# Optimization experiments

Hardware: AMD Instinct MI355X
Metric: run time of the kernel (lower is better)

## Reference

```python
import jax, jax.numpy as jnp
import numpy as np

N_K = 20000; N_E = 50000; N_U = 100000; EMB = 128
E_UND = 200000; E_EK = 400000; E_EU = 600000


def _gat(h, W, a, src, dst, n):
    """RCD GraphLayer: single-head GAT with edge softmax over incoming edges."""
    z = h @ W                                  # [N, d]
    d = z.shape[1]
    el = z @ a[:d]                             # src contribution to attn logit
    er = z @ a[d:]                             # dst contribution
    e = jax.nn.leaky_relu(el[src] + er[dst], 0.01)   # [E]
    m = jax.ops.segment_max(e, dst, num_segments=n)
    m = jnp.where(jnp.isfinite(m), m, 0.0)     # guard zero-degree nodes
    ex = jnp.exp(e - m[dst])
    s = jax.ops.segment_sum(ex, dst, num_segments=n)
    alpha = ex / s[dst]                        # per-dst softmax weights [E]
    return jax.ops.segment_sum(alpha[:, None] * z[src], dst, num_segments=n)


def setup_inputs() -> dict:
    key = jax.random.key(0)
    ks = jax.random.split(key, 32)
    sc = 1.0 / np.sqrt(EMB)
    inp = {
        'kn_emb': jax.random.normal(ks[0], (N_K, EMB), jnp.float32),
        'exer_emb': jax.random.normal(ks[1], (N_E, EMB), jnp.float32),
        'all_stu_emb': jax.random.normal(ks[2], (N_U, EMB), jnp.float32),
        'und_src': jax.random.randint(ks[3], (E_UND,), 0, N_K),
        'und_dst': jax.random.randint(ks[4], (E_UND,), 0, N_K),
        'ek_src': jax.random.randint(ks[5], (E_EK,), 0, N_E),
        'ek_dst': jax.random.randint(ks[6], (E_EK,), 0, N_K),
        'eu_src': jax.random.randint(ks[7], (E_EU,), 0, N_E),
        'eu_dst': jax.random.randint(ks[8], (E_EU,), 0, N_U),
        'W_und': jax.random.normal(ks[9], (EMB, EMB), jnp.float32) * sc,
        'a_und': jax.random.normal(ks[10], (2 * EMB,), jnp.float32) * sc,
        'W_ek': jax.random.normal(ks[11], (EMB, EMB), jnp.float32) * sc,
        'a_ek': jax.random.normal(ks[12], (2 * EMB,), jnp.float32) * sc,
        'W_ke': jax.random.normal(ks[13], (EMB, EMB), jnp.float32) * sc,
        'a_ke': jax.random.normal(ks[14], (2 * EMB,), jnp.float32) * sc,
        'W_eu': jax.random.normal(ks[15], (EMB, EMB), jnp.float32) * sc,
        'a_eu': jax.random.normal(ks[16], (2 * EMB,), jnp.float32) * sc,
        'W_ue': jax.random.normal(ks[17], (EMB, EMB), jnp.float32) * sc,
        'a_ue': jax.random.normal(ks[18], (2 * EMB,), jnp.float32) * sc,
        'k_fc2_w': jax.random.normal(ks[19], (2 * EMB,), jnp.float32) * sc,
        'k_fc2_b': jnp.zeros((1,), jnp.float32),
        'k_fc3_w': jax.random.normal(ks[20], (2 * EMB,), jnp.float32) * sc,
        'k_fc3_b': jnp.zeros((1,), jnp.float32),
        'e_fc1_w': jax.random.normal(ks[21], (2 * EMB,), jnp.float32) * sc,
        'e_fc1_b': jnp.zeros((1,), jnp.float32),
        'e_fc2_w': jax.random.normal(ks[22], (2 * EMB,), jnp.float32) * sc,
        'e_fc2_b': jnp.zeros((1,), jnp.float32),
    }
    return inp


def reference(kn_emb, exer_emb, all_stu_emb, und_src, und_dst, ek_src, ek_dst,
              eu_src, eu_dst, W_und, a_und, W_ek, a_ek, W_ke, a_ke, W_eu, a_eu,
              W_ue, a_ue, k_fc2_w, k_fc2_b, k_fc3_w, k_fc3_b, e_fc1_w, e_fc1_b,
              e_fc2_w, e_fc2_b):
    d = EMB
    # 1) undirected GAT on knowledge graph
    k_und = _gat(kn_emb, W_und, a_und, und_src, und_dst, N_K)
    # 2) exercise<->knowledge graphs on concatenated [exer; kn] nodes
    ek_nodes = jnp.concatenate([exer_emb, kn_emb], axis=0)
    e2k = _gat(ek_nodes, W_ek, a_ek, ek_src, ek_dst + N_E, N_E + N_K)
    k2e = _gat(ek_nodes, W_ke, a_ke, ek_dst + N_E, ek_src, N_E + N_K)
    # 3) exercise<->student graphs on concatenated [exer; stu] nodes
    eu_nodes = jnp.concatenate([exer_emb, all_stu_emb], axis=0)
    e2u = _gat(eu_nodes, W_eu, a_eu, eu_src, eu_dst + N_E, N_E + N_U)
    u2e = _gat(eu_nodes, W_ue, a_ue, eu_dst + N_E, eu_src, N_E + N_U)
    # knowledge fusion: attention-weighted residual combination
    A = kn_emb; C = k_und; D = e2k[N_E:]
    s2 = A @ k_fc2_w[:d] + C @ k_fc2_w[d:] + k_fc2_b[0]
    s3 = A @ k_fc3_w[:d] + D @ k_fc3_w[d:] + k_fc3_b[0]
    sk = jax.nn.softmax(jnp.stack([s2, s3], axis=1), axis=1)
    kn_out = A + sk[:, 0:1] * C + sk[:, 1:2] * D
    # exercise fusion
    Ae = exer_emb; B = k2e[:N_E]; Ce = u2e[:N_E]
    s1 = Ae @ e_fc1_w[:d] + B @ e_fc1_w[d:] + e_fc1_b[0]
    s2e = Ae @ e_fc2_w[:d] + Ce @ e_fc2_w[d:] + e_fc2_b[0]
    se = jax.nn.softmax(jnp.stack([s1, s2e], axis=1), axis=1)
    exer_out = Ae + se[:, 0:1] * B + se[:, 1:2] * Ce
    # student residual
    stu_out = all_stu_emb + e2u[N_E:]
    return (kn_out, exer_out, stu_out)
```

## Files before the change

### kernel.cpp

```cpp
#include <hip/hip_runtime.h>

#define N_K 20000
#define N_E 50000
#define N_U 100000
#define E_TOT 2200000
#define N_TOT 240000
#define KB1 0
#define KB2 20000
#define KB3 40000
#define KB4 90000
#define KB5 190000
#define NBKT 726
#define EPB 8192
#define NBLKA 269
#define APAD 272
#define KN_B 1250
#define EX_B 3125
#define ST_B 6250

typedef unsigned short u16;
typedef unsigned int u32;
typedef __bf16 bf16x8 __attribute__((ext_vector_type(8)));
typedef float f32x4 __attribute__((ext_vector_type(4)));

__device__ __forceinline__ float bf2f(u16 v){
    union { u32 u; float f; } x; x.u = ((u32)v) << 16; return x.f;
}
__device__ __forceinline__ u16 f2bf(float f){
    union { float f; u32 u; } x; x.f = f;
    u32 r = x.u + 0x7FFFu + ((x.u >> 16) & 1u);
    return (u16)(r >> 16);
}
__device__ __forceinline__ float leaky_exp(float x){
    x = x >= 0.f ? x : 0.01f*x;
    return __expf(x);
}

__device__ __forceinline__ int bucket_of(int key){
    if (key < 20000)  return key >> 8;
    if (key < 40000)  return 79  + ((key - 20000) >> 7);
    if (key < 90000)  return 236 + ((key - 40000) >> 9);
    if (key < 190000) return 334 + ((key - 90000) >> 9);
    return 530 + ((key - 190000) >> 8);
}
__device__ __forceinline__ int local_of(int key){
    if (key < 20000)  return key & 255;
    if (key < 40000)  return (key - 20000) & 127;
    if (key < 90000)  return (key - 40000) & 511;
    if (key < 190000) return (key - 90000) & 511;
    return (key - 190000) & 255;
}
__device__ __forceinline__ void bucket_info(int b, int& kb, int& w, int& r){
    if (b < 79){       r=0; kb = b << 8;                 w = min(256, 20000  - kb); }
    else if (b < 236){ r=1; kb = 20000 + ((b-79)  << 7); w = min(128, 40000  - kb); }
    else if (b < 334){ r=2; kb = 40000 + ((b-236) << 9); w = min(512, 90000  - kb); }
    else if (b < 530){ r=3; kb = 90000 + ((b-334) << 9); w = min(512, 190000 - kb); }
    else {             r=4; kb = 190000 + ((b-530) << 8); w = min(256, 240000 - kb); }
}
__device__ __forceinline__ int edge_key(int e,
    const int* ud, const int* es, const int* ed, const int* vs, const int* vd){
    if (e < 200000)  return ud[e];
    if (e < 600000)  return 20000  + ed[e-200000];
    if (e < 1000000) return 40000  + es[e-600000];
    if (e < 1600000) return 90000  + vd[e-1000000];
    return 190000 + vs[e-1600000];
}
__device__ __forceinline__ int edge_src(int e,
    const int* us, const int* es, const int* ed, const int* vs, const int* vd){
    if (e < 200000)  return us[e];
    if (e < 600000)  return es[e-200000];
    if (e < 1000000) return ed[e-600000];
    if (e < 1600000) return vs[e-1000000];
    return vd[e-1600000];
}

__global__ __launch_bounds__(256) void prep_w(
    const float* W0, const float* W1, const float* W2, const float* W3, const float* W4,
    const float* a0, const float* a1, const float* a2, const float* a3, const float* a4,
    float* __restrict__ vecs, u16* __restrict__ Wf)
{
    int bid = blockIdx.x;
    if (bid < 320){
        int o = bid*4 + (threadIdx.x >> 6);
        int lane = threadIdx.x & 63;
        int which = o / 640, rem = o - which*640, g = rem >> 7, k = rem & 127;
        const float* W = g==0?W0:g==1?W1:g==2?W2:g==3?W3:W4;
        const float* a = g==0?a0:g==1?a1:g==2?a2:g==3?a3:a4;
        const float* av = a + which*128;
        int c = lane*2;
        float s = W[k*128 + c]*av[c] + W[k*128 + c + 1]*av[c+1];
        #pragma unroll
        for (int m = 32; m; m >>= 1) s += __shfl_xor(s, m);
        if (lane == 0) vecs[(which*5 + g)*128 + k] = s;
    } else {
        int t = (bid - 320)*256 + threadIdx.x;
        int g = t / 2048, i = t - g*2048;
        const float* W = g==0?W0:g==1?W1:g==2?W2:g==3?W3:W4;
        int lane = i & 63, tt = i >> 6, ks = tt & 3, ct = tt >> 2;
        int kbase = ks*32 + (lane>>4)*8;
        int c = ct*16 + (lane&15);
        #pragma unroll
        for (int j = 0; j < 8; ++j)
            Wf[g*16384 + i*8 + j] = f2bf(W[(kbase+j)*128 + c]);
    }
}

template<int WBF>
__global__ __launch_bounds__(256) void conv_all(
    const float* __restrict__ kn, const float* __restrict__ exer, const float* __restrict__ stu,
    u16* __restrict__ knb, u16* __restrict__ exerb, u16* __restrict__ stub,
    const float* __restrict__ vecs,
    float* __restrict__ el1, float* __restrict__ el2, float* __restrict__ el3,
    float* __restrict__ el4, float* __restrict__ el5, float* __restrict__ erc)
{
    int w = (int)((blockIdx.x*(u32)blockDim.x + threadIdx.x) >> 6);
    int lane = threadIdx.x & 63;
    if (w >= 170000) return;
    const float* h; u16* hb; int local, nd;
    const float *v0,*v1,*v2,*v3;
    float *o0,*o1,*o2,*o3;
    if (w < 20000){
        local = w; h = kn; hb = knb; nd = 4;
        v0=vecs+0;    v1=vecs+640;  v2=vecs+768;  v3=vecs+256;
        o0=el1; o1=erc+KB1; o2=erc+KB2; o3=el3;
    } else if (w < 70000){
        local = w - 20000; h = exer; hb = exerb; nd = 4;
        v0=vecs+128;  v1=vecs+896;  v2=vecs+384;  v3=vecs+1152;
        o0=el2; o1=erc+KB3; o2=el4; o3=erc+KB5;
    } else {
        local = w - 70000; h = stu; hb = stub; nd = 2;
        v0=vecs+1024; v1=vecs+512;  v2=vecs;      v3=vecs;
        o0=erc+KB4; o1=el5; o2=nullptr; o3=nullptr;
    }
    float2 hv = *(const float2*)(h + (size_t)local*128 + lane*2);
    if (WBF)
        *(u32*)(hb + (size_t)local*128 + lane*2) = (u32)f2bf(hv.x) | ((u32)f2bf(hv.y) << 16);
    int c = lane*2;
    float d0 = hv.x*v0[c] + hv.y*v0[c+1];
    float d1 = hv.x*v1[c] + hv.y*v1[c+1];
    float d2 = hv.x*v2[c] + hv.y*v2[c+1];
    float d3 = hv.x*v3[c] + hv.y*v3[c+1];
    #pragma unroll
    for (int o = 32; o; o >>= 1){
        d0 += __shfl_xor(d0, o); d1 += __shfl_xor(d1, o);
        d2 += __shfl_xor(d2, o); d3 += __shfl_xor(d3, o);
    }
    if (lane == 0){
        o0[local] = d0; o1[local] = d1;
        if (nd == 4){ o2[local] = d2; o3[local] = d3; }
    }
}

__global__ __launch_bounds__(256) void bkt_hist(
    const int* __restrict__ ud, const int* __restrict__ es, const int* __restrict__ ed,
    const int* __restrict__ vs, const int* __restrict__ vd, int* __restrict__ hist)
{
    __shared__ int h[NBKT];
    for (int i = threadIdx.x; i < NBKT; i += 256) h[i] = 0;
    __syncthreads();
    int base = blockIdx.x * EPB;
    #pragma unroll 4
    for (int it = 0; it < EPB/256; ++it){
        int e = base + it*256 + threadIdx.x;
        if (e < E_TOT){
            int key = edge_key(e, ud, es, ed, vs, vd);
            atomicAdd(&h[bucket_of(key)], 1);
        }
    }
    __syncthreads();
    for (int i = threadIdx.x; i < NBKT; i += 256)
        hist[i*APAD + blockIdx.x] = h[i];
}

__global__ __launch_bounds__(512) void bkt_scan1(int* __restrict__ hist, int* __restrict__ btot)
{
    __shared__ int sm[512];
    int t = threadIdx.x;
    int v = (t < NBLKA) ? hist[blockIdx.x*APAD + t] : 0;
    sm[t] = v; __syncthreads();
    #pragma unroll
    for (int d = 1; d < 512; d <<= 1){
        int x = (t >= d) ? sm[t-d] : 0;
        __syncthreads();
        sm[t] += x;
        __syncthreads();
    }
    if (t < NBLKA) hist[blockIdx.x*APAD + t] = sm[t] - v;
    if (t == 511) btot[blockIdx.x] = sm[511];
}

__global__ __launch_bounds__(1024) void bkt_scan2(const int* __restrict__ btot, int* __restrict__ bbase)
{
    __shared__ int sm[1024];
    int t = threadIdx.x;
    int v = (t < NBKT) ? btot[t] : 0;
    sm[t] = v; __syncthreads();
    #pragma unroll
    for (int d = 1; d < 1024; d <<= 1){
        int x = (t >= d) ? sm[t-d] : 0;
        __syncthreads();
        sm[t] += x;
        __syncthreads();
    }
    if (t < NBKT) bbase[t] = sm[t] - v;
}

__global__ __launch_bounds__(256) void bkt_scatter(
    const int* __restrict__ us, const int* __restrict__ ud,
    const int* __restrict__ es, const int* __restrict__ ed,
    const int* __restrict__ vs, const int* __restrict__ vd,
    const int* __restrict__ hist, const int* __restrict__ bbase,
    const float* __restrict__ el1, const float* __restrict__ el2,
    const float* __restrict__ el3, const float* __restrict__ el4,
    const float* __restrict__ el5, const float* __restrict__ erc,
    uint2* __restrict__ rec)
{
    __shared__ int cur[NBKT];
    for (int i = threadIdx.x; i < NBKT; i += 256)
        cur[i] = bbase[i] + hist[i*APAD + blockIdx.x];
    __syncthreads();
    int base = blockIdx.x * EPB;
    #pragma unroll 4
    for (int it = 0; it < EPB/256; ++it){
        int e = base + it*256 + threadIdx.x;
        if (e < E_TOT){
            int key = edge_key(e, ud, es, ed, vs, vd);
            int src = edge_src(e, us, es, ed, vs, vd);
            const float* el = (e < 200000) ? el1 : (e < 600000) ? el2 :
                              (e < 1000000) ? el3 : (e < 1600000) ? el4 : el5;
            float ev = leaky_exp(el[src] + erc[key]);
            int local = local_of(key);
            int pos = atomicAdd(&cur[bucket_of(key)], 1);
            rec[pos] = make_uint2((u32)src | ((u32)local << 17), __float_as_uint(ev));
        }
    }
}

__global__ __launch_bounds__(512) void bkt_finalize(const uint2* __restrict__ rec,
    const int* __restrict__ bbase, const int* __restrict__ btot,
    int* __restrict__ cnt, int* __restrict__ offA, int2* __restrict__ sorted2)
{
    __shared__ int   h[512];
    __shared__ float s[512];
    __shared__ int   sm[512];
    __shared__ int   curk[512];
    int b = blockIdx.x, t = threadIdx.x;
    int kb, w, r;
    bucket_info(b, kb, w, r);
    h[t] = 0; s[t] = 0.f;
    __syncthreads();
    int start = bbase[b], n = btot[b];
    for (int i = t; i < n; i += 512){
        uint2 rc = rec[start + i];
        int local = (int)(rc.x >> 17);
        atomicAdd(&h[local], 1);
        atomicAdd(&s[local], __uint_as_float(rc.y));
    }
    __syncthreads();
    int hv = h[t];
    if (t < w) cnt[kb + t] = hv;
    sm[t] = hv; __syncthreads();
    #pragma unroll
    for (int d = 1; d < 512; d <<= 1){
        int x = (t >= d) ? sm[t-d] : 0;
        __syncthreads();
        sm[t] += x;
        __syncthreads();
    }
    int pos0 = start + sm[t] - hv;
    if (t < w) offA[kb + t] = pos0;
    curk[t] = pos0;
    __syncthreads();
    for (int i = t; i < n; i += 512){
        uint2 rc = rec[start + i];
        int local = (int)(rc.x >> 17);
        float alpha = __uint_as_float(rc.y) / s[local];
        int pos = atomicAdd(&curk[local], 1);
        sorted2[pos] = make_int2((int)(rc.x & 0x1FFFFu), __float_as_int(alpha));
    }
}

template<int BF>
__global__ __launch_bounds__(256) void agg_gemm_epi(
    const int* __restrict__ cnt, const int* __restrict__ offA, const int2* __restrict__ sorted2,
    const void* __restrict__ hk, const void* __restrict__ he, const void* __restrict__ hs,
    const u16* __restrict__ Wf,
    const float* __restrict__ kfc2w, const float* __restrict__ kfc2b,
    const float* __restrict__ kfc3w, const float* __restrict__ kfc3b,
    const float* __restrict__ efc1w, const float* __restrict__ efc1b,
    const float* __restrict__ efc2w, const float* __restrict__ efc2b,
    float* __restrict__ out)
{
    __shared__ u16 ldsC[16*136];
    __shared__ u16 ldsD[16*136];
    __shared__ float sred2[16], sred3[16], p2s[16], p3s[16];

    int bid = blockIdx.x;
    int wave = threadIdx.x >> 6, lane = threadIdx.x & 63;
    int g = lane >> 4, s = lane & 15;
    int kind, node0, keyC, keyD;
    const void *hC, *hD, *Aseg;
    const u16 *wc, *wd;
    const float *w2, *b2, *w3, *b3;
    float* outp;
    if (bid < KN_B){
        kind=0; node0 = bid*16;
        keyC = KB1 + node0; keyD = KB2 + node0;
        hC = hk; hD = he; Aseg = hk;
        wc = Wf; wd = Wf + 16384;
        w2=kfc2w; b2=kfc2b; w3=kfc3w; b3=kfc3b;
        outp = out;
    } else if (bid < KN_B + EX_B){
        kind=0; node0 = (bid - KN_B)*16;
        keyC = KB3 + node0; keyD = KB5 + node0;
        hC = hk; hD = hs; Aseg = he;
        wc = Wf + 2*16384; wd = Wf + 4*16384;
        w2=efc1w; b2=efc1b; w3=efc2w; b3=efc2b;
        outp = out + (size_t)N_K*128;
    } else {
        kind=1; node0 = (bid - KN_B - EX_B)*16;
        keyC = KB4 + node0; keyD = 0;
        hC = he; hD = nullptr; Aseg = hs;
        wc = Wf + 3*16384; wd = nullptr;
        w2=nullptr; b2=nullptr; w3=nullptr; b3=nullptr;
        outp = out + (size_t)(N_K + N_E)*128;
    }

    int rpw = (kind == 0) ? 8 : 4;
    for (int rr = 0; rr < rpw; rr += 2){
        int cA = wave*rpw + rr;
        int seg = cA >> 4, ndA = cA & 15;
        int keyA = (seg == 0 ? keyC : keyD) + ndA;
        const u16* hb = (const u16*)(seg == 0 ? hC : hD);
        const float4* hf = (const float4*)(seg == 0 ? hC : hD);
        int degA = cnt[keyA],     startA = offA[keyA];
        int degB = cnt[keyA + 1], startB = offA[keyA + 1];
        float aA8[8], aB8[8];
        #pragma unroll
        for (int k = 0; k < 8; ++k){ aA8[k] = 0.f; aB8[k] = 0.f; }

        auto chunk = [&](const int2* sp, float* acc){
            int2 w = sp[g];
            float al = __int_as_float(w.y);
            if (BF){
                uint4 hv = *(const uint4*)(hb + (size_t)w.x*128 + s*8);
                acc[0] = fmaf(al, bf2f((u16)hv.x), acc[0]);
                acc[1] = fmaf(al, bf2f((u16)(hv.x>>16)), acc[1]);
                acc[2] = fmaf(al, bf2f((u16)hv.y), acc[2]);
                acc[3] = fmaf(al, bf2f((u16)(hv.y>>16)), acc[3]);
                acc[4] = fmaf(al, bf2f((u16)hv.z), acc[4]);
                acc[5] = fmaf(al, bf2f((u16)(hv.z>>16)), acc[5]);
                acc[6] = fmaf(al, bf2f((u16)hv.w), acc[6]);
                acc[7] = fmaf(al, bf2f((u16)(hv.w>>16)), acc[7]);
            } else {
                const float4* rp = hf + (size_t)w.x*32 + s*2;
                float4 p0 = rp[0], p1 = rp[1];
                acc[0] = fmaf(al, p0.x, acc[0]); acc[1] = fmaf(al, p0.y, acc[1]);
                acc[2] = fmaf(al, p0.z, acc[2]); acc[3] = fmaf(al, p0.w, acc[3]);
                acc[4] = fmaf(al, p1.x, acc[4]); acc[5] = fmaf(al, p1.y, acc[5]);
                acc[6] = fmaf(al, p1.z, acc[6]); acc[7] = fmaf(al, p1.w, acc[7]);
            }
        };

        int iA = 0, iB = 0;
        while (iA + 4 <= degA && iB + 4 <= degB){
            chunk(sorted2 + startA + iA, aA8);
            chunk(sorted2 + startB + iB, aB8);
            iA += 4; iB += 4;
        }
        for (; iA + 4 <= degA; iA += 4) chunk(sorted2 + startA + iA, aA8);
        for (; iB + 4 <= degB; iB += 4) chunk(sorted2 + startB + iB, aB8);
        int remA = degA - iA;
        if (g < remA) chunk(sorted2 + startA + iA, aA8);
        int remB = degB - iB;
        if (g < remB) chunk(sorted2 + startB + iB, aB8);

        #pragma unroll
        for (int k = 0; k < 8; ++k){
            aA8[k] += __shfl_xor(aA8[k], 16); aA8[k] += __shfl_xor(aA8[k], 32);
            aB8[k] += __shfl_xor(aB8[k], 16); aB8[k] += __shfl_xor(aB8[k], 32);
        }
        u16* ldsSeg = (seg == 0 ? ldsC : ldsD);
        if (lane < 16){
            u32 p0 = (u32)f2bf(aA8[0]) | ((u32)f2bf(aA8[1]) << 16);
            u32 p1 = (u32)f2bf(aA8[2]) | ((u32)f2bf(aA8[3]) << 16);
            u32 p2 = (u32)f2bf(aA8[4]) | ((u32)f2bf(aA8[5]) << 16);
            u32 p3 = (u32)f2bf(aA8[6]) | ((u32)f2bf(aA8[7]) << 16);
            *(uint4*)(ldsSeg + ndA*136 + lane*8) = make_uint4(p0,p1,p2,p3);
            u32 q0 = (u32)f2bf(aB8[0]) | ((u32)f2bf(aB8[1]) << 16);
            u32 q1 = (u32)f2bf(aB8[2]) | ((u32)f2bf(aB8[3]) << 16);
            u32 q2 = (u32)f2bf(aB8[4]) | ((u32)f2bf(aB8[5]) << 16);
            u32 q3 = (u32)f2bf(aB8[6]) | ((u32)f2bf(aB8[7]) << 16);
            *(uint4*)(ldsSeg + (ndA+1)*136 + lane*8) = make_uint4(q0,q1,q2,q3);
        }
    }
    if (threadIdx.x < 16){ sred2[threadIdx.x] = 0.f; sred3[threadIdx.x] = 0.f; }
    __syncthreads();

    int colb = lane & 15, rlo = (lane >> 4)*4;
    const float* Af = (const float*)Aseg;
    const u16*   Ab = (const u16*)Aseg;

    bf16x8 afC[4];
    #pragma unroll
    for (int ks = 0; ks < 4; ++ks)
        afC[ks] = *(const bf16x8*)(ldsC + (lane & 15)*136 + ks*32 + (lane >> 4)*8);
    f32x4 accC[2];
    accC[0] = (f32x4){0.f,0.f,0.f,0.f}; accC[1] = (f32x4){0.f,0.f,0.f,0.f};
    #pragma unroll
    for (int ci = 0; ci < 2; ++ci){
        int ct = wave*2 + ci;
        #pragma unroll
        for (int ks = 0; ks < 4; ++ks){
            bf16x8 bfr = *(const bf16x8*)(wc + ((ct*4+ks)*64 + lane)*8);
            accC[ci] = __builtin_amdgcn_mfma_f32_16x16x32_bf16(afC[ks], bfr, accC[ci], 0, 0, 0);
        }
    }

    if (kind == 1){
        #pragma unroll
        for (int ci = 0; ci < 2; ++ci){
            int ct = wave*2 + ci;
            #pragma unroll
            for (int j = 0; j < 4; ++j){
                size_t idx = (size_t)(node0 + rlo + j)*128 + ct*16 + colb;
                float av = BF ? bf2f(Ab[idx]) : Af[idx];
                outp[idx] = accC[ci][j] + av;
            }
        }
        return;
    }

    bf16x8 afD[4];
    #pragma unroll
    for (int ks = 0; ks < 4; ++ks)
        afD[ks] = *(const bf16x8*)(ldsD + (lane & 15)*136 + ks*32 + (lane >> 4)*8);
    f32x4 accD[2];
    accD[0] = (f32x4){0.f,0.f,0.f,0.f}; accD[1] = (f32x4){0.f,0.f,0.f,0.f};
    #pragma unroll
    for (int ci = 0; ci < 2; ++ci){
        int ct = wave*2 + ci;
        #pragma unroll
        for (int ks = 0; ks < 4; ++ks){
            bf16x8 bfr = *(const bf16x8*)(wd + ((ct*4+ks)*64 + lane)*8);
            accD[ci] = __builtin_amdgcn_mfma_f32_16x16x32_bf16(afD[ks], bfr, accD[ci], 0, 0, 0);
        }
    }

    float aA[2][4];
    float s2p[4] = {0.f,0.f,0.f,0.f}, s3p[4] = {0.f,0.f,0.f,0.f};
    #pragma unroll
    for (int ci = 0; ci < 2; ++ci){
        int ct = wave*2 + ci;
        float w2l = w2[ct*16 + colb], w2h = w2[128 + ct*16 + colb];
        float w3l = w3[ct*16 + colb], w3h = w3[128 + ct*16 + colb];
        #pragma unroll
        for (int j = 0; j < 4; ++j){
            size_t idx = (size_t)(node0 + rlo + j)*128 + ct*16 + colb;
            float av = BF ? bf2f(Ab[idx]) : Af[idx];
            aA[ci][j] = av;
            s2p[j] = fmaf(av, w2l, fmaf(accC[ci][j], w2h, s2p[j]));
            s3p[j] = fmaf(av, w3l, fmaf(accD[ci][j], w3h, s3p[j]));
        }
    }
    #pragma unroll
    for (int m = 8; m; m >>= 1)
        #pragma unroll
        for (int j = 0; j < 4; ++j){
            s2p[j] += __shfl_xor(s2p[j], m);
            s3p[j] += __shfl_xor(s3p[j], m);
        }
    if (colb == 0){
        #pragma unroll
        for (int j = 0; j < 4; ++j){
            atomicAdd(&sred2[rlo + j], s2p[j]);
            atomicAdd(&sred3[rlo + j], s3p[j]);
        }
    }
    __syncthreads();
    if (threadIdx.x < 16){
        float s2 = sred2[threadIdx.x] + b2[0];
        float s3 = sred3[threadIdx.x] + b3[0];
        float mx = fmaxf(s2, s3);
        float e2 = __expf(s2 - mx), e3 = __expf(s3 - mx);
        float inv = 1.f/(e2 + e3);
        p2s[threadIdx.x] = e2*inv;
        p3s[threadIdx.x] = e3*inv;
    }
    __syncthreads();
    #pragma unroll
    for (int ci = 0; ci < 2; ++ci){
        int ct = wave*2 + ci;
        #pragma unroll
        for (int j = 0; j < 4; ++j){
            int row = rlo + j;
            size_t idx = (size_t)(node0 + row)*128 + ct*16 + colb;
            outp[idx] = aA[ci][j] + p2s[row]*accC[ci][j] + p3s[row]*accD[ci][j];
        }
    }
}

extern "C" void kernel_launch(void* const* d_in, const int* in_sizes, int n_in,
                              void* d_out, int out_size, void* d_ws, size_t ws_size,
                              hipStream_t stream)
{
    (void)in_sizes; (void)n_in; (void)out_size;
    const float* kn   = (const float*)d_in[0];
    const float* exer = (const float*)d_in[1];
    const float* stu  = (const float*)d_in[2];
    const int* und_src = (const int*)d_in[3];
    const int* und_dst = (const int*)d_in[4];
    const int* ek_src  = (const int*)d_in[5];
    const int* ek_dst  = (const int*)d_in[6];
    const int* eu_src  = (const int*)d_in[7];
    const int* eu_dst  = (const int*)d_in[8];
    const float* W_und = (const float*)d_in[9];  const float* a_und = (const float*)d_in[10];
    const float* W_ek  = (const float*)d_in[11]; const float* a_ek  = (const float*)d_in[12];
    const float* W_ke  = (const float*)d_in[13]; const float* a_ke  = (const float*)d_in[14];
    const float* W_eu  = (const float*)d_in[15]; const float* a_eu  = (const float*)d_in[16];
    const float* W_ue  = (const float*)d_in[17]; const float* a_ue  = (const float*)d_in[18];
    const float* kfc2w = (const float*)d_in[19]; const float* kfc2b = (const float*)d_in[20];
    const float* kfc3w = (const float*)d_in[21]; const float* kfc3b = (const float*)d_in[22];
    const float* efc1w = (const float*)d_in[23]; const float* efc1b = (const float*)d_in[24];
    const float* efc2w = (const float*)d_in[25]; const float* efc2b = (const float*)d_in[26];

    char* base = (char*)d_ws;
    size_t off_b = 0;
    auto alloc = [&](size_t bytes)->char*{
        char* p = base + off_b;
        off_b += (bytes + 255) & ~(size_t)255;
        return p;
    };
    float* vecs = (float*)alloc(1280*4);
    u16*   Wf   = (u16*)  alloc(5*16384*2);
    float* el1 = (float*)alloc(N_K*4);
    float* el2 = (float*)alloc(N_E*4);
    float* el3 = (float*)alloc(N_K*4);
    float* el4 = (float*)alloc(N_E*4);
    float* el5 = (float*)alloc(N_U*4);
    float* erc = (float*)alloc((size_t)N_TOT*4);
    int* cnt  = (int*)alloc((size_t)N_TOT*4);
    int* offA = (int*)alloc((size_t)N_TOT*4);
    int* btot = (int*)alloc(NBKT*4);
    int* bbase= (int*)alloc(NBKT*4);
    int* hist = (int*)alloc((size_t)NBKT*APAD*4);
    uint2* rec = (uint2*)alloc((size_t)E_TOT*8);
    int2* sorted2 = (int2*)alloc((size_t)E_TOT*8);
    u16* knb   = (u16*)alloc((size_t)N_K*128*2);
    u16* exerb = (u16*)alloc((size_t)N_E*128*2);
    u16* stub  = (u16*)alloc((size_t)N_U*128*2);
    size_t need_bf = off_b;
    bool useBF = (ws_size >= need_bf);
    float* out = (float*)d_out;

    prep_w<<<360,256,0,stream>>>(W_und,W_ek,W_ke,W_eu,W_ue, a_und,a_ek,a_ke,a_eu,a_ue, vecs, Wf);

    if (useBF)
        conv_all<1><<<(170000+3)/4,256,0,stream>>>(kn, exer, stu, knb, exerb, stub, vecs,
                                                   el1, el2, el3, el4, el5, erc);
    else
        conv_all<0><<<(170000+3)/4,256,0,stream>>>(kn, exer, stu, knb, exerb, stub, vecs,
                                                   el1, el2, el3, el4, el5, erc);

    bkt_hist<<<NBLKA,256,0,stream>>>(und_dst, ek_src, ek_dst, eu_src, eu_dst, hist);
    bkt_scan1<<<NBKT,512,0,stream>>>(hist, btot);
    bkt_scan2<<<1,1024,0,stream>>>(btot, bbase);
    bkt_scatter<<<NBLKA,256,0,stream>>>(und_src, und_dst, ek_src, ek_dst, eu_src, eu_dst,
                                        hist, bbase,
                                        el1, el2, el3, el4, el5, erc, rec);
    bkt_finalize<<<NBKT,512,0,stream>>>(rec, bbase, btot, cnt, offA, sorted2);

    if (useBF){
        agg_gemm_epi<1><<<KN_B+EX_B+ST_B,256,0,stream>>>(cnt, offA, sorted2,
            knb, exerb, stub, Wf,
            kfc2w,kfc2b,kfc3w,kfc3b, efc1w,efc1b,efc2w,efc2b, out);
    } else {
        agg_gemm_epi<0><<<KN_B+EX_B+ST_B,256,0,stream>>>(cnt, offA, sorted2,
            kn, exer, stu, Wf,
            kfc2w,kfc2b,kfc3w,kfc3b, efc1w,efc1b,efc2w,efc2b, out);
    }
}
```

Baseline: 303.4 us.

## Move edge logit computation from scatter into bucket finalize with LDS-cached dst terms

The scatter kernel now writes only the raw src and key per edge, and the attention logit exp is computed in the finalize kernel. There the per-destination term is staged in shared memory for the bucket and the source table is chosen per bucket. This removes random erc gathers and the per-edge segment selects from scatter, at the cost of a new per-edge ev buffer written and reread in finalize. The aggregation loop also gains an 8-wide unrolled interleaved chunk loop to raise memory-level parallelism.

```diff
diff --git a/kernel.cpp b/kernel.cpp
--- a/kernel.cpp
+++ b/kernel.cpp
@@ -42,13 +42,6 @@
     if (key < 90000)  return 236 + ((key - 40000) >> 9);
     if (key < 190000) return 334 + ((key - 90000) >> 9);
     return 530 + ((key - 190000) >> 8);
-}
-__device__ __forceinline__ int local_of(int key){
-    if (key < 20000)  return key & 255;
-    if (key < 40000)  return (key - 20000) & 127;
-    if (key < 90000)  return (key - 40000) & 511;
-    if (key < 190000) return (key - 90000) & 511;
-    return (key - 190000) & 255;
 }
 __device__ __forceinline__ void bucket_info(int b, int& kb, int& w, int& r){
     if (b < 79){       r=0; kb = b << 8;                 w = min(256, 20000  - kb); }
@@ -210,9 +203,6 @@
     const int* __restrict__ es, const int* __restrict__ ed,
     const int* __restrict__ vs, const int* __restrict__ vd,
     const int* __restrict__ hist, const int* __restrict__ bbase,
-    const float* __restrict__ el1, const float* __restrict__ el2,
-    const float* __restrict__ el3, const float* __restrict__ el4,
-    const float* __restrict__ el5, const float* __restrict__ erc,
     uint2* __restrict__ rec)
 {
     __shared__ int cur[NBKT];
@@ -226,35 +216,40 @@
         if (e < E_TOT){
             int key = edge_key(e, ud, es, ed, vs, vd);
             int src = edge_src(e, us, es, ed, vs, vd);
-            const float* el = (e < 200000) ? el1 : (e < 600000) ? el2 :
-                              (e < 1000000) ? el3 : (e < 1600000) ? el4 : el5;
-            float ev = leaky_exp(el[src] + erc[key]);
-            int local = local_of(key);
             int pos = atomicAdd(&cur[bucket_of(key)], 1);
-            rec[pos] = make_uint2((u32)src | ((u32)local << 17), __float_as_uint(ev));
+            rec[pos] = make_uint2((u32)src, (u32)key);
         }
     }
 }
 
 __global__ __launch_bounds__(512) void bkt_finalize(const uint2* __restrict__ rec,
     const int* __restrict__ bbase, const int* __restrict__ btot,
+    const float* __restrict__ erc,
+    const float* __restrict__ el1, const float* __restrict__ el2,
+    const float* __restrict__ el3, const float* __restrict__ el4,
+    const float* __restrict__ el5, float* __restrict__ evb,
     int* __restrict__ cnt, int* __restrict__ offA, int2* __restrict__ sorted2)
 {
     __shared__ int   h[512];
     __shared__ float s[512];
+    __shared__ float ercs[512];
     __shared__ int   sm[512];
     __shared__ int   curk[512];
     int b = blockIdx.x, t = threadIdx.x;
     int kb, w, r;
     bucket_info(b, kb, w, r);
     h[t] = 0; s[t] = 0.f;
-    __syncthreads();
+    if (t < w) ercs[t] = erc[kb + t];
+    __syncthreads();
+    const float* el = r==0?el1 : r==1?el2 : r==2?el3 : r==3?el4 : el5;
     int start = bbase[b], n = btot[b];
     for (int i = t; i < n; i += 512){
         uint2 rc = rec[start + i];
-        int local = (int)(rc.x >> 17);
+        int local = (int)rc.y - kb;
+        float ev = leaky_exp(el[rc.x] + ercs[local]);
+        evb[start + i] = ev;
         atomicAdd(&h[local], 1);
-        atomicAdd(&s[local], __uint_as_float(rc.y));
+        atomicAdd(&s[local], ev);
     }
     __syncthreads();
     int hv = h[t];
@@ -273,10 +268,10 @@
     __syncthreads();
     for (int i = t; i < n; i += 512){
         uint2 rc = rec[start + i];
-        int local = (int)(rc.x >> 17);
-        float alpha = __uint_as_float(rc.y) / s[local];
+        int local = (int)rc.y - kb;
+        float alpha = evb[start + i] / s[local];
         int pos = atomicAdd(&curk[local], 1);
-        sorted2[pos] = make_int2((int)(rc.x & 0x1FFFFu), __float_as_int(alpha));
+        sorted2[pos] = make_int2((int)rc.x, __float_as_int(alpha));
     }
 }
 
@@ -363,6 +358,13 @@
         };
 
         int iA = 0, iB = 0;
+        while (iA + 8 <= degA && iB + 8 <= degB){
+            chunk(sorted2 + startA + iA,     aA8);
+            chunk(sorted2 + startB + iB,     aB8);
+            chunk(sorted2 + startA + iA + 4, aA8);
+            chunk(sorted2 + startB + iB + 4, aB8);
+            iA += 8; iB += 8;
+        }
         while (iA + 4 <= degA && iB + 4 <= degB){
             chunk(sorted2 + startA + iA, aA8);
             chunk(sorted2 + startB + iB, aB8);
@@ -545,6 +547,7 @@
     int* bbase= (int*)alloc(NBKT*4);
     int* hist = (int*)alloc((size_t)NBKT*APAD*4);
     uint2* rec = (uint2*)alloc((size_t)E_TOT*8);
+    float* evb = (float*)alloc((size_t)E_TOT*4);
     int2* sorted2 = (int2*)alloc((size_t)E_TOT*8);
     u16* knb   = (u16*)alloc((size_t)N_K*128*2);
     u16* exerb = (u16*)alloc((size_t)N_E*128*2);
@@ -566,9 +569,10 @@
     bkt_scan1<<<NBKT,512,0,stream>>>(hist, btot);
     bkt_scan2<<<1,1024,0,stream>>>(btot, bbase);
     bkt_scatter<<<NBLKA,256,0,stream>>>(und_src, und_dst, ek_src, ek_dst, eu_src, eu_dst,
-                                        hist, bbase,
-                                        el1, el2, el3, el4, el5, erc, rec);
-    bkt_finalize<<<NBKT,512,0,stream>>>(rec, bbase, btot, cnt, offA, sorted2);
+                                        hist, bbase, rec);
+    bkt_finalize<<<NBKT,512,0,stream>>>(rec, bbase, btot, erc,
+                                        el1, el2, el3, el4, el5, evb,
+                                        cnt, offA, sorted2);
 
     if (useBF){
         agg_gemm_epi<1><<<KN_B+EX_B+ST_B,256,0,stream>>>(cnt, offA, sorted2,
```

Result: faster. 290.9 us (-4.1%).
